# Kernel optimization log

Hardware: AMD Instinct MI355X
Metric: run time of the kernel (lower is better)

## Reference

```python
import jax, jax.numpy as jnp
import numpy as np

N_NODES = 50000


def _gcn_conv(x, W, b, src, dst, n_nodes):
    """PyG GCNConv: add self-loops, D^-1/2 (A+I) D^-1/2 X W + b."""
    loop = jnp.arange(n_nodes, dtype=src.dtype)
    src_f = jnp.concatenate([src, loop])  # [E+N]
    dst_f = jnp.concatenate([dst, loop])
    # degree over destination nodes (edge weight 1, incl. self loops)
    deg = jax.ops.segment_sum(jnp.ones_like(dst_f, dtype=x.dtype), dst_f,
                              num_segments=n_nodes)
    dinv = jnp.where(deg > 0, jax.lax.rsqrt(deg), 0.0)
    norm = dinv[src_f] * dinv[dst_f]  # [E+N]
    h = x @ W  # [N, C_out] dense GEMM first (C_out <= C_in here)
    msg = h[src_f] * norm[:, None]  # gather + scale
    out = jax.ops.segment_sum(msg, dst_f, num_segments=n_nodes)
    return out + b


def setup_inputs() -> dict:
    key = jax.random.key(0)
    k1, k2, k3, k4, k5, k6 = jax.random.split(key, 6)
    in_c, hid_c, out_c = 512, 512, 40
    x = jax.random.normal(k1, (N_NODES, in_c), dtype=jnp.float32)
    edge_index = jax.random.randint(k2, (2, 800000), 0, N_NODES, dtype=jnp.int64)
    # Glorot-style init for the linear weights, zero bias (PyG default)
    W1 = jax.random.normal(k3, (in_c, hid_c), dtype=jnp.float32) / np.sqrt(in_c)
    b1 = jnp.zeros((hid_c,), dtype=jnp.float32)
    W2 = jax.random.normal(k4, (hid_c, out_c), dtype=jnp.float32) / np.sqrt(hid_c)
    b2 = jnp.zeros((out_c,), dtype=jnp.float32)
    return {"x": x, "edge_index": edge_index, "W1": W1, "b1": b1,
            "W2": W2, "b2": b2}


def reference(x, edge_index, W1, b1, W2, b2):
    src, dst = edge_index[0], edge_index[1]
    h = _gcn_conv(x, W1, b1, src, dst, N_NODES)
    h = jax.nn.relu(h)
    h = _gcn_conv(h, W2, b2, src, dst, N_NODES)
    return jax.nn.log_softmax(h, axis=1)
```

## Files before the change

### kernel.cpp

```cpp
#include <hip/hip_runtime.h>


typedef unsigned int u32;
typedef unsigned short u16;
typedef __bf16 bf16x8 __attribute__((ext_vector_type(8)));
typedef float f32x4 __attribute__((ext_vector_type(4)));
typedef u32 u32x4 __attribute__((ext_vector_type(4)));

#define C_IN 512
#define C_HID 512
#define C_OUT 40
#define H_SCALE 24.0f
#define H_INV_SCALE (1.0f / 24.0f)

__device__ __forceinline__ float bf2f(u16 u) {
    u32 x = ((u32)u) << 16;
    return __builtin_bit_cast(float, x);
}
__device__ __forceinline__ u16 f2bf(float f) {
    u32 x = __builtin_bit_cast(u32, f);
    x += 0x7fffu + ((x >> 16) & 1u);
    return (u16)(x >> 16);
}
__device__ __forceinline__ char q8(float v) {
    float c = fminf(fmaxf(v * H_SCALE, -127.f), 127.f);
    return (char)__float2int_rn(c);
}
__device__ __forceinline__ u32 pk2(float a, float b) {
    u16 lo = __builtin_bit_cast(u16, (__bf16)a);
    u16 hi = __builtin_bit_cast(u16, (__bf16)b);
    return (u32)lo | ((u32)hi << 16);
}
__device__ __forceinline__ u32x4 pk8(float4 a, float4 b) {
    u32x4 r;
    r.x = pk2(a.x, a.y); r.y = pk2(a.z, a.w);
    r.z = pk2(b.x, b.y); r.w = pk2(b.z, b.w);
    return r;
}
__host__ __device__ __forceinline__ int imin(int a, int b) { return a < b ? a : b; }
__host__ __device__ __forceinline__ int imax(int a, int b) { return a > b ? a : b; }

__global__ void k_init(const u32* __restrict__ x32, const int* __restrict__ ei,
                       int* flags, int* deg, int* cursor, int n) {
    if (blockIdx.x == 0 && threadIdx.x < 64) {
        int lane = threadIdx.x;
        int z = (ei[2 * lane + 1] == 0) ? 1 : 0;
        u32 e = (x32[lane] >> 7) & 0xff;
        int v = (e >= 110 && e <= 133) ? 1 : 0;
        unsigned long long bz = __ballot(z);
        unsigned long long bv = __ballot(v);
        if (lane == 0) {
            flags[0] = (__popcll(bz) == 64) ? 2 : 1;
            flags[1] = (__popcll(bv) >= 48) ? 1 : 0;
        }
    }
    int i = blockIdx.x * 256 + threadIdx.x;
    if (i < n) { deg[i] = 1; cursor[i] = 0; }
}

__global__ void k_deg(const int* __restrict__ ei, const int* __restrict__ flags,
                      int* deg, int E, int ecap, int n) {
    int e = blockIdx.x * 256 + threadIdx.x;
    if (e >= E) return;
    int st = flags[0];
    int cap = ecap * st - 1;
    u32 d = (u32)ei[imin((E + e) * st, cap)];
    if (d < (u32)n) atomicAdd(&deg[d], 1);
}

__global__ void k_scanA(const int* __restrict__ deg, int* bsum, float* dinv, int n) {
    __shared__ int sh[256];
    int i = blockIdx.x * 256 + threadIdx.x;
    int dv = (i < n) ? deg[i] : 1;
    if (i < n) dinv[i] = rsqrtf((float)imax(dv, 1));
    sh[threadIdx.x] = (i < n) ? dv - 1 : 0;
    __syncthreads();
    for (int d = 128; d > 0; d >>= 1) {
        if (threadIdx.x < d) sh[threadIdx.x] += sh[threadIdx.x + d];
        __syncthreads();
    }
    if (threadIdx.x == 0) bsum[blockIdx.x] = sh[0];
}

__global__ void k_scanB(int* bsum, int nb, int* offs, int n) {
    __shared__ int sh[256];
    int t = threadIdx.x;
    int carry = 0;
    for (int base = 0; base < nb; base += 256) {
        int i = base + t;
        int v = (i < nb) ? bsum[i] : 0;
        sh[t] = v;
        __syncthreads();
        for (int d = 1; d < 256; d <<= 1) {
            int add = (t >= d) ? sh[t - d] : 0;
            __syncthreads();
            sh[t] += add;
            __syncthreads();
        }
        if (i < nb) bsum[i] = carry + sh[t] - v;
        int tot = sh[255];
        __syncthreads();
        carry += tot;
    }
    if (t == 0) offs[n] = carry;
}

__global__ void k_scanC(const int* __restrict__ deg, const int* __restrict__ bsum,
                        int* offs, int n) {
    __shared__ int sh[256];
    int t = threadIdx.x;
    int i = blockIdx.x * 256 + t;
    int v = (i < n) ? deg[i] - 1 : 0;
    sh[t] = v;
    __syncthreads();
    for (int d = 1; d < 256; d <<= 1) {
        int add = (t >= d) ? sh[t - d] : 0;
        __syncthreads();
        sh[t] += add;
        __syncthreads();
    }
    if (i < n) offs[i] = bsum[blockIdx.x] + sh[t] - v;
}

__global__ void k_sort(const int* __restrict__ ei, const int* __restrict__ flags,
                       const int* __restrict__ offs, int* cursor, int* csr,
                       int E, int ecap, int n) {
    int e = blockIdx.x * 256 + threadIdx.x;
    if (e >= E) return;
    int st = flags[0];
    int cap = ecap * st - 1;
    u32 d = (u32)ei[imin((E + e) * st, cap)];
    u32 s = (u32)ei[imin(e * st, cap)];
    if (d < (u32)n && s < (u32)n) {
        int pos = offs[d] + atomicAdd(&cursor[(int)d], 1);
        if ((u32)pos < (u32)E) csr[pos] = (int)s;
    }
}

__device__ __forceinline__ float ldf(const void* p, int i, int isbf) {
    return isbf ? bf2f(((const u16*)p)[i]) : ((const float*)p)[i];
}

__global__ __launch_bounds__(256) void k_prep(
    const void* __restrict__ W1, const void* __restrict__ b1,
    const void* __restrict__ W2, const void* __restrict__ b2,
    const int* __restrict__ flags, u16* __restrict__ w1t, u16* __restrict__ w2t,
    float* __restrict__ b1f, float* __restrict__ b2f) {
    int isbf = flags[1];
    int stride = gridDim.x * 256;
    int i0 = blockIdx.x * 256 + threadIdx.x;
    for (int i = i0; i < 512 * 512; i += stride) {
        int n = i >> 9, k = i & 511;
        w1t[n * 512 + k] = f2bf(ldf(W1, k * 512 + n, isbf));
    }
    for (int i = i0; i < 64 * 512; i += stride) {
        int n = i >> 9, k = i & 511;
        w2t[i] = (n < C_OUT) ? f2bf(ldf(W2, k * C_OUT + n, isbf)) : (u16)0;
    }
    if (i0 < C_HID) b1f[i0] = ldf(b1, i0, isbf);
    if (i0 < C_OUT) b2f[i0] = ldf(b2, i0, isbf);
}

typedef __attribute__((address_space(1))) const u32 glds_src;
typedef __attribute__((address_space(3))) u32 glds_dst;

__global__ __launch_bounds__(256) void k_gemm128(
    const u16* __restrict__ xbf, const float* __restrict__ xf32,
    const int* __restrict__ flags, const u16* __restrict__ Bt,
    char* __restrict__ C, int M, int K, int ldc) {
    int isbf = flags[1];
    __shared__ __align__(16) u16 As0[64 * 32], As1[64 * 32];
    __shared__ __align__(16) u16 Bs0[128 * 32], Bs1[128 * 32];
    int tid = threadIdx.x;
    int wave = tid >> 6, lane = tid & 63;
    int quad = lane >> 4, lrow = lane & 15;
    int wrow = (wave & 1) * 32, wcol = (wave >> 1) * 64;

    int nwg = gridDim.x;
    int id = blockIdx.x;
    int q = nwg >> 3, r = nwg & 7;
    int xcd = id & 7, j8 = id >> 3;
    int wg = (xcd < r ? xcd * (q + 1) : r * (q + 1) + (xcd - r) * q) + j8;
    int row0 = (wg >> 2) * 64;
    int n0 = (wg & 3) * 128;

    int lr = lane >> 2;
    int lc = (lane & 3) * 8;
    int ar = row0 + wave * 16 + lr;
    int br = n0 + wave * 32 + lr;
    u16* As0_w = As0 + (wave * 16) * 32;
    u16* As1_w = As1 + (wave * 16) * 32;
    u16* Bs0_w = Bs0 + (wave * 32) * 32;
    u16* Bs1_w = Bs1 + (wave * 32) * 32;

    f32x4 acc[2][4] = {};
    int kTiles = K >> 6;
    for (int kt = 0; kt < kTiles; ++kt) {
        int k0 = kt * 64;
        int a0 = imin(ar, M - 1);
        if (isbf) {
            const u16* gA0 = xbf + (size_t)a0 * K + k0 + lc;
            __builtin_amdgcn_global_load_lds((glds_src*)gA0, (glds_dst*)As0_w, 16, 0, 0);
            __builtin_amdgcn_global_load_lds((glds_src*)(gA0 + 32), (glds_dst*)As1_w, 16, 0, 0);
        } else {
            const float* f0 = xf32 + (size_t)a0 * K + k0 + lc;
            float4 u0 = *(const float4*)(f0);
            float4 u1 = *(const float4*)(f0 + 4);
            float4 u2 = *(const float4*)(f0 + 32);
            float4 u3 = *(const float4*)(f0 + 36);
            *(u32x4*)(As0_w + lr * 32 + lc) = pk8(u0, u1);
            *(u32x4*)(As1_w + lr * 32 + lc) = pk8(u2, u3);
        }
        const u16* gB0 = Bt + (size_t)br * K + k0 + lc;
        const u16* gB1 = Bt + (size_t)(br + 16) * K + k0 + lc;
        __builtin_amdgcn_global_load_lds((glds_src*)gB0, (glds_dst*)Bs0_w, 16, 0, 0);
        __builtin_amdgcn_global_load_lds((glds_src*)gB1, (glds_dst*)(Bs0_w + 16 * 32), 16, 0, 0);
        __builtin_amdgcn_global_load_lds((glds_src*)(gB0 + 32), (glds_dst*)Bs1_w, 16, 0, 0);
        __builtin_amdgcn_global_load_lds((glds_src*)(gB1 + 32), (glds_dst*)(Bs1_w + 16 * 32), 16, 0, 0);
        __syncthreads();
#pragma unroll
        for (int ko = 0; ko < 2; ++ko) {
            const u16* Asrc = ko ? As1 : As0;
            const u16* Bsrc = ko ? Bs1 : Bs0;
            bf16x8 af[2], bfr[4];
#pragma unroll
            for (int i = 0; i < 2; ++i)
                af[i] = *(const bf16x8*)(Asrc + (wrow + i * 16 + lrow) * 32 + quad * 8);
#pragma unroll
            for (int j = 0; j < 4; ++j)
                bfr[j] = *(const bf16x8*)(Bsrc + (wcol + j * 16 + lrow) * 32 + quad * 8);
#pragma unroll
            for (int i = 0; i < 2; ++i)
#pragma unroll
                for (int j = 0; j < 4; ++j)
                    acc[i][j] = __builtin_amdgcn_mfma_f32_16x16x32_bf16(af[i], bfr[j],
                                                                        acc[i][j], 0, 0, 0);
        }
        __syncthreads();
    }
#pragma unroll
    for (int i = 0; i < 2; ++i)
#pragma unroll
        for (int j = 0; j < 4; ++j)
#pragma unroll
            for (int r2 = 0; r2 < 4; ++r2) {
                int row = row0 + wrow + i * 16 + quad * 4 + r2;
                int col = n0 + wcol + j * 16 + lrow;
                if (row < M) C[(size_t)row * ldc + col] = q8(acc[i][j][r2]);
            }
}

__global__ __launch_bounds__(256) void k_gemm64(
    const u16* __restrict__ A, const u16* __restrict__ Bt, u16* __restrict__ Cout,
    int M, int K, int Ncols, int ldc) {
    __shared__ __align__(16) u16 As[64 * 32];
    __shared__ __align__(16) u16 Bs[64 * 32];
    int tid = threadIdx.x;
    int wave = tid >> 6, lane = tid & 63;
    int quad = lane >> 4, lrow = lane & 15;
    int row0 = blockIdx.x * 64;
    int n0 = blockIdx.y * 64;
    int srow = tid >> 2;
    int skc = (tid & 3) * 8;

    f32x4 acc[4] = {};
    int kTiles = K >> 5;
    for (int kt = 0; kt < kTiles; ++kt) {
        int k0 = kt * 32;
        uint4 av = make_uint4(0, 0, 0, 0);
        int gr = row0 + srow;
        if (gr < M) av = *(const uint4*)(A + (size_t)gr * K + k0 + skc);
        uint4 bv = *(const uint4*)(Bt + (size_t)(n0 + srow) * K + k0 + skc);
        __syncthreads();
        *(uint4*)(As + srow * 32 + skc) = av;
        *(uint4*)(Bs + srow * 32 + skc) = bv;
        __syncthreads();
        bf16x8 af = *(const bf16x8*)(As + (wave * 16 + lrow) * 32 + quad * 8);
#pragma unroll
        for (int t = 0; t < 4; ++t) {
            bf16x8 bfr = *(const bf16x8*)(Bs + (t * 16 + lrow) * 32 + quad * 8);
            acc[t] = __builtin_amdgcn_mfma_f32_16x16x32_bf16(af, bfr, acc[t], 0, 0, 0);
        }
    }
#pragma unroll
    for (int t = 0; t < 4; ++t)
#pragma unroll
        for (int r = 0; r < 4; ++r) {
            int row = wave * 16 + quad * 4 + r;
            int col = t * 16 + lrow;
            int gr = row0 + row, gc = n0 + col;
            if (gr < M && gc < Ncols) Cout[(size_t)gr * ldc + gc] = f2bf(acc[t][r]);
        }
}

__device__ __forceinline__ void accum8i(float* acc, uint2 p, float w) {
    int lo = (int)p.x, hi = (int)p.y;
    acc[0] += w * (float)(signed char)(lo);
    acc[1] += w * (float)(signed char)(lo >> 8);
    acc[2] += w * (float)(signed char)(lo >> 16);
    acc[3] += w * (float)(signed char)(lo >> 24);
    acc[4] += w * (float)(signed char)(hi);
    acc[5] += w * (float)(signed char)(hi >> 8);
    acc[6] += w * (float)(signed char)(hi >> 16);
    acc[7] += w * (float)(signed char)(hi >> 24);
}

__global__ __launch_bounds__(256) void k_agg1(
    const char* __restrict__ hq, const int* __restrict__ csr, const int* __restrict__ offs,
    const float* __restrict__ dinv, const float* __restrict__ b1f,
    u16* __restrict__ out, int n, int Etot) {
    int wave = threadIdx.x >> 6, lane = threadIdx.x & 63;
    int v = blockIdx.x * 4 + wave;
    if (v >= n) return;
    float dv = dinv[v];
    float wself = dv * dv * H_INV_SCALE;

    float acc[8] = {0.f, 0.f, 0.f, 0.f, 0.f, 0.f, 0.f, 0.f};
    uint2 hs = *(const uint2*)(hq + (size_t)v * C_HID + lane * 8);
    accum8i(acc, hs, wself);

    int e0 = imax(0, imin(offs[v], Etot));
    int e1 = imax(e0, imin(offs[v + 1], Etot));
    for (int base = e0; base < e1; base += 64) {
        int cnt = imin(64, e1 - base);
        int sreg = 0; float wreg = 0.f;
        if (lane < cnt) {
            u32 s = (u32)csr[base + lane];
            s = (s < (u32)n) ? s : 0u;
            sreg = (int)s;
            wreg = dv * dinv[s] * H_INV_SCALE;
        }
        int j = 0;
        for (; j + 16 <= cnt; j += 16) {
            int ss[16]; float ww[16]; uint2 pp[16];
#pragma unroll
            for (int t = 0; t < 16; ++t) {
                ss[t] = __shfl(sreg, j + t);
                ww[t] = __shfl(wreg, j + t);
            }
#pragma unroll
            for (int t = 0; t < 16; ++t)
                pp[t] = *(const uint2*)(hq + (size_t)ss[t] * C_HID + lane * 8);
#pragma unroll
            for (int t = 0; t < 16; ++t) accum8i(acc, pp[t], ww[t]);
        }
        for (; j + 8 <= cnt; j += 8) {
            int ss[8]; float ww[8]; uint2 pp[8];
#pragma unroll
            for (int t = 0; t < 8; ++t) {
                ss[t] = __shfl(sreg, j + t);
                ww[t] = __shfl(wreg, j + t);
            }
#pragma unroll
            for (int t = 0; t < 8; ++t)
                pp[t] = *(const uint2*)(hq + (size_t)ss[t] * C_HID + lane * 8);
#pragma unroll
            for (int t = 0; t < 8; ++t) accum8i(acc, pp[t], ww[t]);
        }
        for (; j + 4 <= cnt; j += 4) {
            int ss[4]; float ww[4]; uint2 pp[4];
#pragma unroll
            for (int t = 0; t < 4; ++t) {
                ss[t] = __shfl(sreg, j + t);
                ww[t] = __shfl(wreg, j + t);
            }
#pragma unroll
            for (int t = 0; t < 4; ++t)
                pp[t] = *(const uint2*)(hq + (size_t)ss[t] * C_HID + lane * 8);
#pragma unroll
            for (int t = 0; t < 4; ++t) accum8i(acc, pp[t], ww[t]);
        }
        for (; j < cnt; ++j) {
            int sj = __shfl(sreg, j);
            float wj = __shfl(wreg, j);
            uint2 pj = *(const uint2*)(hq + (size_t)sj * C_HID + lane * 8);
            accum8i(acc, pj, wj);
        }
    }

    float4 ba = *(const float4*)(b1f + lane * 8);
    float4 bb = *(const float4*)(b1f + lane * 8 + 4);
    float r0 = fmaxf(acc[0] + ba.x, 0.f), r1 = fmaxf(acc[1] + ba.y, 0.f);
    float r2 = fmaxf(acc[2] + ba.z, 0.f), r3 = fmaxf(acc[3] + ba.w, 0.f);
    float r4 = fmaxf(acc[4] + bb.x, 0.f), r5 = fmaxf(acc[5] + bb.y, 0.f);
    float r6 = fmaxf(acc[6] + bb.z, 0.f), r7 = fmaxf(acc[7] + bb.w, 0.f);
    u32x4 o;
    o.x = (u32)f2bf(r0) | ((u32)f2bf(r1) << 16);
    o.y = (u32)f2bf(r2) | ((u32)f2bf(r3) << 16);
    o.z = (u32)f2bf(r4) | ((u32)f2bf(r5) << 16);
    o.w = (u32)f2bf(r6) | ((u32)f2bf(r7) << 16);
    __builtin_nontemporal_store(o, (u32x4*)(out + (size_t)v * C_HID + lane * 8));
}

__global__ __launch_bounds__(256) void k_agg2(
    const u16* __restrict__ h2, const int* __restrict__ csr, const int* __restrict__ offs,
    const float* __restrict__ dinv, const float* __restrict__ b2f,
    const int* __restrict__ flags, void* __restrict__ out, int n, int Etot) {
    int wave = threadIdx.x >> 6, lane = threadIdx.x & 63;
    int v = blockIdx.x * 4 + wave;
    if (v >= n) return;
    float dv = dinv[v];

    int g = lane / 10;
    int f4 = lane - g * 10;
    bool active = (g < 6);

    float4 acc = make_float4(0.f, 0.f, 0.f, 0.f);
    if (g == 0) {
        uint2 pv = *(const uint2*)(h2 + (size_t)v * C_OUT + f4 * 4);
        float w = dv * dv;
        acc.x = w * bf2f((u16)pv.x); acc.y = w * bf2f((u16)(pv.x >> 16));
        acc.z = w * bf2f((u16)pv.y); acc.w = w * bf2f((u16)(pv.y >> 16));
    }

    int e0 = imax(0, imin(offs[v], Etot));
    int e1 = imax(e0, imin(offs[v + 1], Etot));
    for (int base = e0; base < e1; base += 64) {
        int cnt = imin(64, e1 - base);
        int sreg = 0; float wreg = 0.f;
        if (lane < cnt) {
            u32 s = (u32)csr[base + lane];
            s = (s < (u32)n) ? s : 0u;
            sreg = (int)s;
            wreg = dv * dinv[s];
        }
        for (int j = 0; j < cnt; j += 24) {
            uint2 p[4]; float w4[4];
#pragma unroll
            for (int t = 0; t < 4; ++t) {
                int jj = j + t * 6 + g;
                int idx = imin(jj, cnt - 1);
                int sj = __shfl(sreg, idx);
                float wj = __shfl(wreg, idx);
                w4[t] = (active && jj < cnt) ? wj : 0.f;
                p[t] = make_uint2(0, 0);
                if (active) p[t] = *(const uint2*)(h2 + (size_t)sj * C_OUT + f4 * 4);
            }
#pragma unroll
            for (int t = 0; t < 4; ++t) {
                acc.x += w4[t] * bf2f((u16)p[t].x);
                acc.y += w4[t] * bf2f((u16)(p[t].x >> 16));
                acc.z += w4[t] * bf2f((u16)p[t].y);
                acc.w += w4[t] * bf2f((u16)(p[t].y >> 16));
            }
        }
    }

    float4 t;
    t.x = __shfl(acc.x, lane + 30); t.y = __shfl(acc.y, lane + 30);
    t.z = __shfl(acc.z, lane + 30); t.w = __shfl(acc.w, lane + 30);
    if (lane < 30) { acc.x += t.x; acc.y += t.y; acc.z += t.z; acc.w += t.w; }
    float4 t1, t2;
    t1.x = __shfl(acc.x, lane + 10); t1.y = __shfl(acc.y, lane + 10);
    t1.z = __shfl(acc.z, lane + 10); t1.w = __shfl(acc.w, lane + 10);
    t2.x = __shfl(acc.x, lane + 20); t2.y = __shfl(acc.y, lane + 20);
    t2.z = __shfl(acc.z, lane + 20); t2.w = __shfl(acc.w, lane + 20);
    if (lane < 10) {
        acc.x += t1.x + t2.x; acc.y += t1.y + t2.y;
        acc.z += t1.z + t2.z; acc.w += t1.w + t2.w;
        acc.x += b2f[f4 * 4 + 0]; acc.y += b2f[f4 * 4 + 1];
        acc.z += b2f[f4 * 4 + 2]; acc.w += b2f[f4 * 4 + 3];
    }

    float m = -1e30f;
    if (lane < 10) m = fmaxf(fmaxf(acc.x, acc.y), fmaxf(acc.z, acc.w));
    for (int off = 32; off > 0; off >>= 1) m = fmaxf(m, __shfl_xor(m, off));
    float s = 0.f;
    if (lane < 10)
        s = expf(acc.x - m) + expf(acc.y - m) + expf(acc.z - m) + expf(acc.w - m);
    for (int off = 32; off > 0; off >>= 1) s += __shfl_xor(s, off);
    if (lane < 10) {
        float ls = m + logf(s);
        if (flags[1]) {
            ushort4 o;
            o.x = f2bf(acc.x - ls); o.y = f2bf(acc.y - ls);
            o.z = f2bf(acc.z - ls); o.w = f2bf(acc.w - ls);
            *(ushort4*)((u16*)out + (size_t)v * C_OUT + f4 * 4) = o;
        } else {
            float4 o = make_float4(acc.x - ls, acc.y - ls, acc.z - ls, acc.w - ls);
            *(float4*)((float*)out + (size_t)v * C_OUT + f4 * 4) = o;
        }
    }
}


extern "C" void kernel_launch(void* const* d_in, const int* in_sizes, int n_in,
                              void* d_out, int out_size, void* d_ws, size_t ws_size,
                              hipStream_t stream) {
    const void* x = d_in[0];
    const int* ei = (const int*)d_in[1];
    const void* W1 = d_in[2];
    const void* b1 = d_in[3];
    const void* W2 = d_in[4];
    const void* b2 = d_in[5];

    const int N = out_size / C_OUT;
    const int Mx = in_sizes[0] / C_IN;
    const int M = (N < Mx) ? N : Mx;
    const int ECAP = in_sizes[1];
    const int E = ECAP / 2;

    char* p = (char*)d_ws;
    size_t used = 0;
    auto carve = [&](size_t bytes) -> void* {
        void* r = (void*)p;
        size_t b = (bytes + 255) & ~(size_t)255;
        p += b; used += b;
        return r;
    };
    int* flags = (int*)carve(256);
    int* deg = (int*)carve((size_t)N * 4);
    int* cursor = (int*)carve((size_t)N * 4);
    float* dinv = (float*)carve((size_t)N * 4);
    int* offs = (int*)carve((size_t)(N + 1) * 4);
    int* bsum = (int*)carve(8192);
    int* csr = (int*)carve((size_t)E * 4);
    u16* w1t = (u16*)carve((size_t)C_HID * C_IN * 2);
    u16* w2t = (u16*)carve((size_t)64 * C_HID * 2);
    float* b1f = (float*)carve(C_HID * 4);
    float* b2f = (float*)carve(256);
    u16* bufA = (u16*)carve((size_t)N * C_HID * 2);
    u16* bufB = (u16*)carve((size_t)N * C_HID * 2);
    if (used > ws_size) return;

    char* h_i8 = (char*)bufB;
    u16* hagg = bufA;
    u16* h2 = bufB;

    const int NB = (N + 255) / 256;
    const int EB = (E + 255) / 256;

    k_init<<<NB, 256, 0, stream>>>((const u32*)x, ei, flags, deg, cursor, N);
    k_deg<<<EB, 256, 0, stream>>>(ei, flags, deg, E, ECAP, N);
    k_scanA<<<NB, 256, 0, stream>>>(deg, bsum, dinv, N);
    k_scanB<<<1, 256, 0, stream>>>(bsum, NB, offs, N);
    k_scanC<<<NB, 256, 0, stream>>>(deg, bsum, offs, N);
    k_sort<<<EB, 256, 0, stream>>>(ei, flags, offs, cursor, csr, E, ECAP, N);

    k_prep<<<256, 256, 0, stream>>>(W1, b1, W2, b2, flags, w1t, w2t, b1f, b2f);

    int nbx = (M + 63) / 64;
    k_gemm128<<<nbx * 4, 256, 0, stream>>>((const u16*)x, (const float*)x, flags,
                                           w1t, h_i8, M, C_IN, C_HID);

    k_agg1<<<(N + 3) / 4, 256, 0, stream>>>(h_i8, csr, offs, dinv, b1f, hagg, N, E);

    dim3 g2((N + 63) / 64, 1);
    k_gemm64<<<g2, 256, 0, stream>>>(hagg, w2t, h2, N, C_HID, C_OUT, C_OUT);

    k_agg2<<<(N + 3) / 4, 256, 0, stream>>>(h2, csr, offs, dinv, b2f, flags, d_out, N, E);
}
```

Baseline: 400.3 us.

## Double-buffer LDS and prefetch next fp32 A tile in first-layer GEMM

Restructures the 128-wide GEMM main loop to use two LDS buffer sets alternating by k-tile, with a single barrier per iteration instead of two. For fp32 input, the next tile's A values are loaded into registers while the current tile is staged and computed, using explicit waitcnt and sched_barrier to keep the prefetch loads in flight. The aim is to hide global load latency behind MFMA work. LDS usage doubles, which could reduce occupancy, and the hand-written vmcnt counts are fragile.

```diff
diff --git a/kernel.cpp b/kernel.cpp
--- a/kernel.cpp
+++ b/kernel.cpp
@@ -169,8 +169,8 @@
     const int* __restrict__ flags, const u16* __restrict__ Bt,
     char* __restrict__ C, int M, int K, int ldc) {
     int isbf = flags[1];
-    __shared__ __align__(16) u16 As0[64 * 32], As1[64 * 32];
-    __shared__ __align__(16) u16 Bs0[128 * 32], Bs1[128 * 32];
+    __shared__ __align__(16) u16 As[2][2][64 * 32];
+    __shared__ __align__(16) u16 Bs[2][2][128 * 32];
     int tid = threadIdx.x;
     int wave = tid >> 6, lane = tid & 63;
     int quad = lane >> 4, lrow = lane & 15;
@@ -188,40 +188,61 @@
     int lc = (lane & 3) * 8;
     int ar = row0 + wave * 16 + lr;
     int br = n0 + wave * 32 + lr;
-    u16* As0_w = As0 + (wave * 16) * 32;
-    u16* As1_w = As1 + (wave * 16) * 32;
-    u16* Bs0_w = Bs0 + (wave * 32) * 32;
-    u16* Bs1_w = Bs1 + (wave * 32) * 32;
+    int a0 = imin(ar, M - 1);
+    const float* fbase = xf32 + (size_t)a0 * K + lc;
+    const u16* bbase = xbf + (size_t)a0 * K + lc;
+    const u16* gB0b = Bt + (size_t)br * K + lc;
+    const u16* gB1b = Bt + (size_t)(br + 16) * K + lc;
 
     f32x4 acc[2][4] = {};
     int kTiles = K >> 6;
+
+    float4 r0, r1, r2, r3;
+    if (!isbf) {
+        const float* f = fbase;
+        r0 = *(const float4*)(f);      r1 = *(const float4*)(f + 4);
+        r2 = *(const float4*)(f + 32); r3 = *(const float4*)(f + 36);
+    }
+
     for (int kt = 0; kt < kTiles; ++kt) {
-        int k0 = kt * 64;
-        int a0 = imin(ar, M - 1);
+        int b = kt & 1;
+        u16* A0w = &As[b][0][(wave * 16) * 32];
+        u16* A1w = &As[b][1][(wave * 16) * 32];
+        u16* B0w = &Bs[b][0][(wave * 32) * 32];
+        u16* B1w = &Bs[b][1][(wave * 32) * 32];
+        __syncthreads();
         if (isbf) {
-            const u16* gA0 = xbf + (size_t)a0 * K + k0 + lc;
-            __builtin_amdgcn_global_load_lds((glds_src*)gA0, (glds_dst*)As0_w, 16, 0, 0);
-            __builtin_amdgcn_global_load_lds((glds_src*)(gA0 + 32), (glds_dst*)As1_w, 16, 0, 0);
+            const u16* g = bbase + kt * 64;
+            __builtin_amdgcn_global_load_lds((glds_src*)g, (glds_dst*)A0w, 16, 0, 0);
+            __builtin_amdgcn_global_load_lds((glds_src*)(g + 32), (glds_dst*)A1w, 16, 0, 0);
         } else {
-            const float* f0 = xf32 + (size_t)a0 * K + k0 + lc;
-            float4 u0 = *(const float4*)(f0);
-            float4 u1 = *(const float4*)(f0 + 4);
-            float4 u2 = *(const float4*)(f0 + 32);
-            float4 u3 = *(const float4*)(f0 + 36);
-            *(u32x4*)(As0_w + lr * 32 + lc) = pk8(u0, u1);
-            *(u32x4*)(As1_w + lr * 32 + lc) = pk8(u2, u3);
-        }
-        const u16* gB0 = Bt + (size_t)br * K + k0 + lc;
-        const u16* gB1 = Bt + (size_t)(br + 16) * K + k0 + lc;
-        __builtin_amdgcn_global_load_lds((glds_src*)gB0, (glds_dst*)Bs0_w, 16, 0, 0);
-        __builtin_amdgcn_global_load_lds((glds_src*)gB1, (glds_dst*)(Bs0_w + 16 * 32), 16, 0, 0);
-        __builtin_amdgcn_global_load_lds((glds_src*)(gB0 + 32), (glds_dst*)Bs1_w, 16, 0, 0);
-        __builtin_amdgcn_global_load_lds((glds_src*)(gB1 + 32), (glds_dst*)(Bs1_w + 16 * 32), 16, 0, 0);
-        __syncthreads();
+            *(u32x4*)(A0w + lr * 32 + lc) = pk8(r0, r1);
+            *(u32x4*)(A1w + lr * 32 + lc) = pk8(r2, r3);
+        }
+        const u16* g0 = gB0b + kt * 64;
+        const u16* g1 = gB1b + kt * 64;
+        __builtin_amdgcn_global_load_lds((glds_src*)g0, (glds_dst*)B0w, 16, 0, 0);
+        __builtin_amdgcn_global_load_lds((glds_src*)g1, (glds_dst*)(B0w + 16 * 32), 16, 0, 0);
+        __builtin_amdgcn_global_load_lds((glds_src*)(g0 + 32), (glds_dst*)B1w, 16, 0, 0);
+        __builtin_amdgcn_global_load_lds((glds_src*)(g1 + 32), (glds_dst*)(B1w + 16 * 32), 16, 0, 0);
+        bool pre = (!isbf) && (kt + 1 < kTiles);
+        if (pre) {
+            __builtin_amdgcn_sched_barrier(0);
+            const float* f = fbase + (kt + 1) * 64;
+            r0 = *(const float4*)(f);      r1 = *(const float4*)(f + 4);
+            r2 = *(const float4*)(f + 32); r3 = *(const float4*)(f + 36);
+            __builtin_amdgcn_sched_barrier(0);
+            asm volatile("s_waitcnt vmcnt(4) lgkmcnt(0)" ::: "memory");
+        } else {
+            asm volatile("s_waitcnt vmcnt(0) lgkmcnt(0)" ::: "memory");
+        }
+        __builtin_amdgcn_sched_barrier(0);
+        __builtin_amdgcn_s_barrier();
+        __builtin_amdgcn_sched_barrier(0);
 #pragma unroll
         for (int ko = 0; ko < 2; ++ko) {
-            const u16* Asrc = ko ? As1 : As0;
-            const u16* Bsrc = ko ? Bs1 : Bs0;
+            const u16* Asrc = &As[b][ko][0];
+            const u16* Bsrc = &Bs[b][ko][0];
             bf16x8 af[2], bfr[4];
 #pragma unroll
             for (int i = 0; i < 2; ++i)
@@ -236,17 +257,16 @@
                     acc[i][j] = __builtin_amdgcn_mfma_f32_16x16x32_bf16(af[i], bfr[j],
                                                                         acc[i][j], 0, 0, 0);
         }
-        __syncthreads();
     }
 #pragma unroll
     for (int i = 0; i < 2; ++i)
 #pragma unroll
         for (int j = 0; j < 4; ++j)
 #pragma unroll
-            for (int r2 = 0; r2 < 4; ++r2) {
-                int row = row0 + wrow + i * 16 + quad * 4 + r2;
+            for (int r2i = 0; r2i < 4; ++r2i) {
+                int row = row0 + wrow + i * 16 + quad * 4 + r2i;
                 int col = n0 + wcol + j * 16 + lrow;
-                if (row < M) C[(size_t)row * ldc + col] = q8(acc[i][j][r2]);
+                if (row < M) C[(size_t)row * ldc + col] = q8(acc[i][j][r2i]);
             }
 }
 
```

After: 414.3 us. 3.5% more time.

## Load GEMM fragments directly from global memory, bypassing LDS staging

Applied to the files above, without the earlier changes.

The first-layer GEMM stops staging A and B tiles through shared memory with barriers. Each wave now loads its MFMA fragments straight from global memory into registers, converting fp32 to bf16 inline when needed. This removes the LDS round trip and the syncthreads calls. In exchange, waves that share a tile reload the same data, so there is less cross-wave reuse and more global/L2 traffic.

```diff
diff --git a/kernel.cpp b/kernel.cpp
--- a/kernel.cpp
+++ b/kernel.cpp
@@ -31,11 +31,11 @@
     u16 hi = __builtin_bit_cast(u16, (__bf16)b);
     return (u32)lo | ((u32)hi << 16);
 }
-__device__ __forceinline__ u32x4 pk8(float4 a, float4 b) {
+__device__ __forceinline__ bf16x8 pkfrag(float4 a, float4 b) {
     u32x4 r;
     r.x = pk2(a.x, a.y); r.y = pk2(a.z, a.w);
     r.z = pk2(b.x, b.y); r.w = pk2(b.z, b.w);
-    return r;
+    return __builtin_bit_cast(bf16x8, r);
 }
 __host__ __device__ __forceinline__ int imin(int a, int b) { return a < b ? a : b; }
 __host__ __device__ __forceinline__ int imax(int a, int b) { return a > b ? a : b; }
@@ -161,16 +161,11 @@
     if (i0 < C_OUT) b2f[i0] = ldf(b2, i0, isbf);
 }
 
-typedef __attribute__((address_space(1))) const u32 glds_src;
-typedef __attribute__((address_space(3))) u32 glds_dst;
-
 __global__ __launch_bounds__(256) void k_gemm128(
     const u16* __restrict__ xbf, const float* __restrict__ xf32,
     const int* __restrict__ flags, const u16* __restrict__ Bt,
     char* __restrict__ C, int M, int K, int ldc) {
     int isbf = flags[1];
-    __shared__ __align__(16) u16 As0[64 * 32], As1[64 * 32];
-    __shared__ __align__(16) u16 Bs0[128 * 32], Bs1[128 * 32];
     int tid = threadIdx.x;
     int wave = tid >> 6, lane = tid & 63;
     int quad = lane >> 4, lrow = lane & 15;
@@ -184,69 +179,68 @@
     int row0 = (wg >> 2) * 64;
     int n0 = (wg & 3) * 128;
 
-    int lr = lane >> 2;
-    int lc = (lane & 3) * 8;
-    int ar = row0 + wave * 16 + lr;
-    int br = n0 + wave * 32 + lr;
-    u16* As0_w = As0 + (wave * 16) * 32;
-    u16* As1_w = As1 + (wave * 16) * 32;
-    u16* Bs0_w = Bs0 + (wave * 32) * 32;
-    u16* Bs1_w = Bs1 + (wave * 32) * 32;
+    int r0i = imin(row0 + wrow + lrow, M - 1);
+    int r1i = imin(row0 + wrow + 16 + lrow, M - 1);
+    const float* aF0 = xf32 + (size_t)r0i * K + quad * 8;
+    const float* aF1 = xf32 + (size_t)r1i * K + quad * 8;
+    const u16* aB0 = xbf + (size_t)r0i * K + quad * 8;
+    const u16* aB1 = xbf + (size_t)r1i * K + quad * 8;
+    const u16* bP0 = Bt + (size_t)(n0 + wcol + 0 * 16 + lrow) * K + quad * 8;
+    const u16* bP1 = Bt + (size_t)(n0 + wcol + 1 * 16 + lrow) * K + quad * 8;
+    const u16* bP2 = Bt + (size_t)(n0 + wcol + 2 * 16 + lrow) * K + quad * 8;
+    const u16* bP3 = Bt + (size_t)(n0 + wcol + 3 * 16 + lrow) * K + quad * 8;
 
     f32x4 acc[2][4] = {};
-    int kTiles = K >> 6;
-    for (int kt = 0; kt < kTiles; ++kt) {
-        int k0 = kt * 64;
-        int a0 = imin(ar, M - 1);
-        if (isbf) {
-            const u16* gA0 = xbf + (size_t)a0 * K + k0 + lc;
-            __builtin_amdgcn_global_load_lds((glds_src*)gA0, (glds_dst*)As0_w, 16, 0, 0);
-            __builtin_amdgcn_global_load_lds((glds_src*)(gA0 + 32), (glds_dst*)As1_w, 16, 0, 0);
-        } else {
-            const float* f0 = xf32 + (size_t)a0 * K + k0 + lc;
-            float4 u0 = *(const float4*)(f0);
-            float4 u1 = *(const float4*)(f0 + 4);
-            float4 u2 = *(const float4*)(f0 + 32);
-            float4 u3 = *(const float4*)(f0 + 36);
-            *(u32x4*)(As0_w + lr * 32 + lc) = pk8(u0, u1);
-            *(u32x4*)(As1_w + lr * 32 + lc) = pk8(u2, u3);
-        }
-        const u16* gB0 = Bt + (size_t)br * K + k0 + lc;
-        const u16* gB1 = Bt + (size_t)(br + 16) * K + k0 + lc;
-        __builtin_amdgcn_global_load_lds((glds_src*)gB0, (glds_dst*)Bs0_w, 16, 0, 0);
-        __builtin_amdgcn_global_load_lds((glds_src*)gB1, (glds_dst*)(Bs0_w + 16 * 32), 16, 0, 0);
-        __builtin_amdgcn_global_load_lds((glds_src*)(gB0 + 32), (glds_dst*)Bs1_w, 16, 0, 0);
-        __builtin_amdgcn_global_load_lds((glds_src*)(gB1 + 32), (glds_dst*)(Bs1_w + 16 * 32), 16, 0, 0);
-        __syncthreads();
-#pragma unroll
-        for (int ko = 0; ko < 2; ++ko) {
-            const u16* Asrc = ko ? As1 : As0;
-            const u16* Bsrc = ko ? Bs1 : Bs0;
-            bf16x8 af[2], bfr[4];
-#pragma unroll
-            for (int i = 0; i < 2; ++i)
-                af[i] = *(const bf16x8*)(Asrc + (wrow + i * 16 + lrow) * 32 + quad * 8);
-#pragma unroll
-            for (int j = 0; j < 4; ++j)
-                bfr[j] = *(const bf16x8*)(Bsrc + (wcol + j * 16 + lrow) * 32 + quad * 8);
-#pragma unroll
-            for (int i = 0; i < 2; ++i)
-#pragma unroll
-                for (int j = 0; j < 4; ++j)
-                    acc[i][j] = __builtin_amdgcn_mfma_f32_16x16x32_bf16(af[i], bfr[j],
-                                                                        acc[i][j], 0, 0, 0);
-        }
-        __syncthreads();
+    if (isbf) {
+#pragma unroll 4
+        for (int k0 = 0; k0 < C_IN; k0 += 32) {
+            bf16x8 a0 = *(const bf16x8*)(aB0 + k0);
+            bf16x8 a1 = *(const bf16x8*)(aB1 + k0);
+            bf16x8 b0 = *(const bf16x8*)(bP0 + k0);
+            bf16x8 b1 = *(const bf16x8*)(bP1 + k0);
+            bf16x8 b2 = *(const bf16x8*)(bP2 + k0);
+            bf16x8 b3 = *(const bf16x8*)(bP3 + k0);
+            acc[0][0] = __builtin_amdgcn_mfma_f32_16x16x32_bf16(a0, b0, acc[0][0], 0, 0, 0);
+            acc[0][1] = __builtin_amdgcn_mfma_f32_16x16x32_bf16(a0, b1, acc[0][1], 0, 0, 0);
+            acc[0][2] = __builtin_amdgcn_mfma_f32_16x16x32_bf16(a0, b2, acc[0][2], 0, 0, 0);
+            acc[0][3] = __builtin_amdgcn_mfma_f32_16x16x32_bf16(a0, b3, acc[0][3], 0, 0, 0);
+            acc[1][0] = __builtin_amdgcn_mfma_f32_16x16x32_bf16(a1, b0, acc[1][0], 0, 0, 0);
+            acc[1][1] = __builtin_amdgcn_mfma_f32_16x16x32_bf16(a1, b1, acc[1][1], 0, 0, 0);
+            acc[1][2] = __builtin_amdgcn_mfma_f32_16x16x32_bf16(a1, b2, acc[1][2], 0, 0, 0);
+            acc[1][3] = __builtin_amdgcn_mfma_f32_16x16x32_bf16(a1, b3, acc[1][3], 0, 0, 0);
+        }
+    } else {
+#pragma unroll 4
+        for (int k0 = 0; k0 < C_IN; k0 += 32) {
+            float4 u0 = *(const float4*)(aF0 + k0);
+            float4 u1 = *(const float4*)(aF0 + k0 + 4);
+            float4 u2 = *(const float4*)(aF1 + k0);
+            float4 u3 = *(const float4*)(aF1 + k0 + 4);
+            bf16x8 b0 = *(const bf16x8*)(bP0 + k0);
+            bf16x8 b1 = *(const bf16x8*)(bP1 + k0);
+            bf16x8 b2 = *(const bf16x8*)(bP2 + k0);
+            bf16x8 b3 = *(const bf16x8*)(bP3 + k0);
+            bf16x8 a0 = pkfrag(u0, u1);
+            bf16x8 a1 = pkfrag(u2, u3);
+            acc[0][0] = __builtin_amdgcn_mfma_f32_16x16x32_bf16(a0, b0, acc[0][0], 0, 0, 0);
+            acc[0][1] = __builtin_amdgcn_mfma_f32_16x16x32_bf16(a0, b1, acc[0][1], 0, 0, 0);
+            acc[0][2] = __builtin_amdgcn_mfma_f32_16x16x32_bf16(a0, b2, acc[0][2], 0, 0, 0);
+            acc[0][3] = __builtin_amdgcn_mfma_f32_16x16x32_bf16(a0, b3, acc[0][3], 0, 0, 0);
+            acc[1][0] = __builtin_amdgcn_mfma_f32_16x16x32_bf16(a1, b0, acc[1][0], 0, 0, 0);
+            acc[1][1] = __builtin_amdgcn_mfma_f32_16x16x32_bf16(a1, b1, acc[1][1], 0, 0, 0);
+            acc[1][2] = __builtin_amdgcn_mfma_f32_16x16x32_bf16(a1, b2, acc[1][2], 0, 0, 0);
+            acc[1][3] = __builtin_amdgcn_mfma_f32_16x16x32_bf16(a1, b3, acc[1][3], 0, 0, 0);
+        }
     }
 #pragma unroll
     for (int i = 0; i < 2; ++i)
 #pragma unroll
         for (int j = 0; j < 4; ++j)
 #pragma unroll
-            for (int r2 = 0; r2 < 4; ++r2) {
-                int row = row0 + wrow + i * 16 + quad * 4 + r2;
+            for (int r2i = 0; r2i < 4; ++r2i) {
+                int row = row0 + wrow + i * 16 + quad * 4 + r2i;
                 int col = n0 + wcol + j * 16 + lrow;
-                if (row < M) C[(size_t)row * ldc + col] = q8(acc[i][j][r2]);
+                if (row < M) C[(size_t)row * ldc + col] = q8(acc[i][j][r2i]);
             }
 }
 
```

Result: slower. 528.6 us (+32.0%).

## Stage whole W2 in LDS for second GEMM and tile-transpose W1 in prep

Applied to the files above, without the earlier changes.

The second GEMM now loads the 48 live output columns of the transposed W2 into padded shared memory once per block. Each wave then streams A rows straight from global memory, covering 32 rows against 3 column tiles with no per-k-step barriers. This drops the padded 64-column tile and the two syncthreads per K step, at the cost of uncoalesced per-lane A loads and larger LDS use. The W1 transpose in prep now goes through a shared-memory tile so that both reads and writes are coalesced.

```diff
diff --git a/kernel.cpp b/kernel.cpp
--- a/kernel.cpp
+++ b/kernel.cpp
@@ -146,12 +146,22 @@
     const void* __restrict__ W2, const void* __restrict__ b2,
     const int* __restrict__ flags, u16* __restrict__ w1t, u16* __restrict__ w2t,
     float* __restrict__ b1f, float* __restrict__ b2f) {
+    __shared__ float tile[64][65];
     int isbf = flags[1];
+    int tid = threadIdx.x;
     int stride = gridDim.x * 256;
-    int i0 = blockIdx.x * 256 + threadIdx.x;
-    for (int i = i0; i < 512 * 512; i += stride) {
-        int n = i >> 9, k = i & 511;
-        w1t[n * 512 + k] = f2bf(ldf(W1, k * 512 + n, isbf));
+    int i0 = blockIdx.x * 256 + tid;
+    for (int t = blockIdx.x; t < 64; t += gridDim.x) {
+        int tr = t >> 3, tc = t & 7;
+        int rr = tid >> 2, cq = (tid & 3) * 16;
+#pragma unroll
+        for (int c = 0; c < 16; ++c)
+            tile[cq + c][rr] = ldf(W1, (tr * 64 + rr) * 512 + tc * 64 + cq + c, isbf);
+        __syncthreads();
+#pragma unroll
+        for (int c = 0; c < 16; ++c)
+            w1t[(size_t)(tc * 64 + rr) * 512 + tr * 64 + cq + c] = f2bf(tile[rr][cq + c]);
+        __syncthreads();
     }
     for (int i = i0; i < 64 * 512; i += stride) {
         int n = i >> 9, k = i & 511;
@@ -250,47 +260,58 @@
             }
 }
 
+#define B2ROW 520
 __global__ __launch_bounds__(256) void k_gemm64(
     const u16* __restrict__ A, const u16* __restrict__ Bt, u16* __restrict__ Cout,
     int M, int K, int Ncols, int ldc) {
-    __shared__ __align__(16) u16 As[64 * 32];
-    __shared__ __align__(16) u16 Bs[64 * 32];
+    __shared__ __align__(16) u16 Bsh[48 * B2ROW];
     int tid = threadIdx.x;
     int wave = tid >> 6, lane = tid & 63;
     int quad = lane >> 4, lrow = lane & 15;
-    int row0 = blockIdx.x * 64;
-    int n0 = blockIdx.y * 64;
-    int srow = tid >> 2;
-    int skc = (tid & 3) * 8;
-
-    f32x4 acc[4] = {};
-    int kTiles = K >> 5;
-    for (int kt = 0; kt < kTiles; ++kt) {
-        int k0 = kt * 32;
-        uint4 av = make_uint4(0, 0, 0, 0);
-        int gr = row0 + srow;
-        if (gr < M) av = *(const uint4*)(A + (size_t)gr * K + k0 + skc);
-        uint4 bv = *(const uint4*)(Bt + (size_t)(n0 + srow) * K + k0 + skc);
-        __syncthreads();
-        *(uint4*)(As + srow * 32 + skc) = av;
-        *(uint4*)(Bs + srow * 32 + skc) = bv;
-        __syncthreads();
-        bf16x8 af = *(const bf16x8*)(As + (wave * 16 + lrow) * 32 + quad * 8);
-#pragma unroll
-        for (int t = 0; t < 4; ++t) {
-            bf16x8 bfr = *(const bf16x8*)(Bs + (t * 16 + lrow) * 32 + quad * 8);
-            acc[t] = __builtin_amdgcn_mfma_f32_16x16x32_bf16(af, bfr, acc[t], 0, 0, 0);
-        }
-    }
-#pragma unroll
-    for (int t = 0; t < 4; ++t)
-#pragma unroll
-        for (int r = 0; r < 4; ++r) {
-            int row = wave * 16 + quad * 4 + r;
-            int col = t * 16 + lrow;
-            int gr = row0 + row, gc = n0 + col;
-            if (gr < M && gc < Ncols) Cout[(size_t)gr * ldc + gc] = f2bf(acc[t][r]);
-        }
+
+    for (int i = tid; i < 48 * 64; i += 256) {
+        int rw = i >> 6, cv = (i & 63) * 8;
+        *(uint4*)(Bsh + rw * B2ROW + cv) = *(const uint4*)(Bt + (size_t)rw * 512 + cv);
+    }
+    __syncthreads();
+
+    int row0 = blockIdx.x * 128 + wave * 32;
+    int r0 = imin(row0 + lrow, M - 1);
+    int r1 = imin(row0 + 16 + lrow, M - 1);
+    const u16* a0p = A + (size_t)r0 * K + quad * 8;
+    const u16* a1p = A + (size_t)r1 * K + quad * 8;
+    const u16* b0p = Bsh + (0 * 16 + lrow) * B2ROW + quad * 8;
+    const u16* b1p = Bsh + (1 * 16 + lrow) * B2ROW + quad * 8;
+    const u16* b2p = Bsh + (2 * 16 + lrow) * B2ROW + quad * 8;
+
+    f32x4 c00 = {}, c01 = {}, c02 = {};
+    f32x4 c10 = {}, c11 = {}, c12 = {};
+#pragma unroll 4
+    for (int k0 = 0; k0 < C_HID; k0 += 32) {
+        bf16x8 a0 = *(const bf16x8*)(a0p + k0);
+        bf16x8 a1 = *(const bf16x8*)(a1p + k0);
+        bf16x8 b0 = *(const bf16x8*)(b0p + k0);
+        bf16x8 b1 = *(const bf16x8*)(b1p + k0);
+        bf16x8 b2 = *(const bf16x8*)(b2p + k0);
+        c00 = __builtin_amdgcn_mfma_f32_16x16x32_bf16(a0, b0, c00, 0, 0, 0);
+        c01 = __builtin_amdgcn_mfma_f32_16x16x32_bf16(a0, b1, c01, 0, 0, 0);
+        c02 = __builtin_amdgcn_mfma_f32_16x16x32_bf16(a0, b2, c02, 0, 0, 0);
+        c10 = __builtin_amdgcn_mfma_f32_16x16x32_bf16(a1, b0, c10, 0, 0, 0);
+        c11 = __builtin_amdgcn_mfma_f32_16x16x32_bf16(a1, b1, c11, 0, 0, 0);
+        c12 = __builtin_amdgcn_mfma_f32_16x16x32_bf16(a1, b2, c12, 0, 0, 0);
+    }
+    f32x4 cc[2][3] = {{c00, c01, c02}, {c10, c11, c12}};
+#pragma unroll
+    for (int i = 0; i < 2; ++i)
+#pragma unroll
+        for (int t = 0; t < 3; ++t)
+#pragma unroll
+            for (int r = 0; r < 4; ++r) {
+                int row = row0 + i * 16 + quad * 4 + r;
+                int col = t * 16 + lrow;
+                if (row < M && col < Ncols)
+                    Cout[(size_t)row * ldc + col] = f2bf(cc[i][t][r]);
+            }
 }
 
 __device__ __forceinline__ void accum8i(float* acc, uint2 p, float w) {
@@ -545,8 +566,7 @@
 
     k_agg1<<<(N + 3) / 4, 256, 0, stream>>>(h_i8, csr, offs, dinv, b1f, hagg, N, E);
 
-    dim3 g2((N + 63) / 64, 1);
-    k_gemm64<<<g2, 256, 0, stream>>>(hagg, w2t, h2, N, C_HID, C_OUT, C_OUT);
+    k_gemm64<<<(M + 127) / 128, 256, 0, stream>>>(hagg, w2t, h2, N, C_HID, C_OUT, C_OUT);
 
     k_agg2<<<(N + 3) / 4, 256, 0, stream>>>(h2, csr, offs, dinv, b2f, flags, d_out, N, E);
 }
```

After: 404.5 us. No clear change (+1.1%).
